# Kernel tuning notes

Hardware: AMD Instinct MI355X
Metric: run time of the kernel (lower is better)

## Reference

```python
import jax, jax.numpy as jnp
import numpy as np

NUM_USER = 100000
NUM_ITEM = 50000
N = NUM_USER + NUM_ITEM
E = 1200000
D = 64          # emb_size
F_ITEM = 384    # raw item multimodal feature dim
K = 3           # number of global embedding rows (summed over dim 0)
N_LAYERS = 4
EPS = 1e-8      # F.cosine_similarity default eps


def setup_inputs() -> dict:
    key = jax.random.key(0)
    ks = jax.random.split(key, 9)
    return {
        "adj_row": jax.random.randint(ks[0], (E,), 0, N),
        "adj_col": jax.random.randint(ks[1], (E,), 0, N),
        # scaled like a degree-normalized adjacency (avg degree ~8)
        "adj_val": jax.random.uniform(ks[2], (E,), jnp.float32) / 8.0,
        "user_fea": jax.random.normal(ks[3], (NUM_USER, D), jnp.float32) * 0.1,
        "item_fea": jax.random.normal(ks[4], (NUM_ITEM, F_ITEM), jnp.float32) * 0.1,
        "g_emb_u": jax.random.normal(ks[5], (K, D), jnp.float32) * 0.1,
        "g_emb_i": jax.random.normal(ks[6], (K, D), jnp.float32) * 0.1,
        "mlp_w": jax.random.normal(ks[7], (D, F_ITEM), jnp.float32) * (1.0 / np.sqrt(F_ITEM)),
        "mlp_b": jnp.zeros((D,), jnp.float32),
    }


def _cosine_sim(a, b):
    # matches F.cosine_similarity(a, b, dim=-1) with eps clamp on norms
    na = jnp.maximum(jnp.linalg.norm(a, axis=-1), EPS)
    nb = jnp.maximum(jnp.linalg.norm(b, axis=-1), EPS)
    return jnp.sum(a * b, axis=-1) / (na * nb)


def reference(adj_row, adj_col, adj_val, user_fea, item_fea, g_emb_u, g_emb_i, mlp_w, mlp_b):
    # global embeddings summed over modality dim
    user_emb = user_fea + jnp.sum(g_emb_u, axis=0)                       # [U, D]
    item_emb = jnp.tanh(item_fea @ mlp_w.T + mlp_b) + jnp.sum(g_emb_i, axis=0)  # [I, D]
    ego = jnp.concatenate([user_emb, item_emb], axis=0)                  # [N, D]

    x = ego
    acc = ego  # sum over layers, includes layer-0 (ego) term
    for _ in range(N_LAYERS):
        # sparse adj @ x as gather -> scale -> segment-sum scatter
        x = jax.ops.segment_sum(adj_val[:, None] * x[adj_col], adj_row, num_segments=N)
        w = _cosine_sim(x, ego)     # [N]
        x = w[:, None] * x          # einsum('a,ab->ab')
        acc = acc + x

    return acc[:NUM_USER], acc[NUM_USER:]
```

## Files before the change

kernel.cpp:

```cpp
#include <hip/hip_runtime.h>
#include <hip/hip_bf16.h>

#define U_NUM 100000
#define I_NUM 50000
#define N_NUM 150000
#define E_NUM 1200000
#define D 64
#define F_IT 384
#define CAP 32
#define EPSV 1e-8f

typedef unsigned short ushort_t;
typedef unsigned int uint_t;
typedef short bf16x8 __attribute__((ext_vector_type(8)));
typedef float f32x4 __attribute__((ext_vector_type(4)));

__device__ __forceinline__ ushort_t f2bf(float f) {
    uint_t x = __float_as_uint(f);
    uint_t r = x + 0x7fffu + ((x >> 16) & 1u);
    return (ushort_t)(r >> 16);
}
__device__ __forceinline__ float bfu2f(uint_t u_lo16) {
    return __uint_as_float(u_lo16 << 16);
}

__global__ void k_zero(int* p, int n) {
    int i = blockIdx.x * 256 + threadIdx.x;
    if (i < n) p[i] = 0;
}

__global__ void k_fill(const int* __restrict__ row, const int* __restrict__ col,
                       const float* __restrict__ val,
                       int* __restrict__ cnt, int2* __restrict__ bkt) {
    int t = blockIdx.x * 256 + threadIdx.x;
    if (t >= E_NUM / 4) return;
    int r[4], c[4];
    float v[4];
#pragma unroll
    for (int k = 0; k < 4; k++) {
        int e = t + k * (E_NUM / 4);
        r[k] = row[e]; c[k] = col[e]; v[k] = val[e];
    }
    int p[4];
#pragma unroll
    for (int k = 0; k < 4; k++) p[k] = atomicAdd(&cnt[r[k]], 1);
#pragma unroll
    for (int k = 0; k < 4; k++) {
        if (p[k] < CAP) bkt[r[k] * CAP + p[k]] = make_int2(c[k], __float_as_int(v[k]));
    }
}

__global__ void k_wcast(const float* __restrict__ w, short* __restrict__ wbf) {
    int i = blockIdx.x * 256 + threadIdx.x;
    wbf[i] = (short)f2bf(w[i]);
}

__global__ void k_user(const float* __restrict__ ufea, const float* __restrict__ gu,
                       float* __restrict__ ego, ushort_t* __restrict__ egob) {
    int i = blockIdx.x * 256 + threadIdx.x;
    int d = i & 63;
    float g = gu[d] + gu[64 + d] + gu[128 + d];
    float v = ufea[i] + g;
    ego[i] = v;
    egob[i] = f2bf(v);
}

__global__ __launch_bounds__(256) void k_item(const float* __restrict__ ifea,
                                              const short* __restrict__ wbf,
                                              const float* __restrict__ b,
                                              const float* __restrict__ gi,
                                              float* __restrict__ ego,
                                              ushort_t* __restrict__ egob) {
    int wave = threadIdx.x >> 6;
    int lane = threadIdx.x & 63;
    int q = lane >> 4, m = lane & 15;
    int ibase = blockIdx.x * 64 + wave * 16;

    int irow = min(ibase + m, I_NUM - 1);
    const float* arow = ifea + (size_t)irow * F_IT + q * 8;

    f32x4 av[4];
#pragma unroll
    for (int n = 0; n < 4; n++) av[n] = (f32x4){0.f, 0.f, 0.f, 0.f};

#pragma unroll
    for (int c = 0; c < 12; c++) {
        float4 fa0 = ((const float4*)(arow + c * 32))[0];
        float4 fa1 = ((const float4*)(arow + c * 32))[1];
        bf16x8 af;
        af[0] = (short)f2bf(fa0.x); af[1] = (short)f2bf(fa0.y);
        af[2] = (short)f2bf(fa0.z); af[3] = (short)f2bf(fa0.w);
        af[4] = (short)f2bf(fa1.x); af[5] = (short)f2bf(fa1.y);
        af[6] = (short)f2bf(fa1.z); af[7] = (short)f2bf(fa1.w);
#pragma unroll
        for (int n = 0; n < 4; n++) {
            bf16x8 bf = *(const bf16x8*)(wbf + (size_t)(n * 16 + m) * F_IT + c * 32 + q * 8);
            av[n] = __builtin_amdgcn_mfma_f32_16x16x32_bf16(af, bf, av[n], 0, 0, 0);
        }
    }

#pragma unroll
    for (int n = 0; n < 4; n++) {
        int dim = n * 16 + m;
        float bb = b[dim];
        float gg = gi[dim] + gi[64 + dim] + gi[128 + dim];
#pragma unroll
        for (int r = 0; r < 4; r++) {
            int item = ibase + q * 4 + r;
            if (item < I_NUM) {
                float v = tanhf(av[n][r] + bb) + gg;
                size_t o = (size_t)(U_NUM + item) * D + dim;
                ego[o] = v;
                egob[o] = f2bf(v);
            }
        }
    }
}

__global__ void k_norm(const float* __restrict__ ego, float* __restrict__ nrm) {
    int t = blockIdx.x * 256 + threadIdx.x;
    int r = t >> 4, l = t & 15;
    float4 e = ((const float4*)ego)[r * 16 + l];
    float s = e.x * e.x + e.y * e.y + e.z * e.z + e.w * e.w;
    s += __shfl_xor(s, 1);
    s += __shfl_xor(s, 2);
    s += __shfl_xor(s, 4);
    s += __shfl_xor(s, 8);
    if (l == 0) nrm[r] = fmaxf(sqrtf(s), EPSV);
}

__global__ __launch_bounds__(256) void k_spmm(const ushort_t* __restrict__ xb,
                                              const ushort_t* __restrict__ egob,
                                              const float* __restrict__ nrm,
                                              const int* __restrict__ cnt,
                                              const int2* __restrict__ bkt,
                                              ushort_t* __restrict__ xob) {
    int t = blockIdx.x * 256 + threadIdx.x;
    int r = t >> 3, l = t & 7;
    if (r >= N_NUM) return;
    int deg = min(cnt[r], CAP);
    const int2* bp = bkt + (size_t)r * CAP;

    int2 eb0 = bp[l], eb1 = bp[l + 8], eb2 = bp[l + 16], eb3 = bp[l + 24];

    float a[8];
#pragma unroll
    for (int j = 0; j < 8; j++) a[j] = 0.f;

    int nch = (deg + 7) >> 3;
    for (int k = 0; k < nch; k++) {
        int2 e = (k == 0) ? eb0 : (k == 1) ? eb1 : (k == 2) ? eb2 : eb3;
#pragma unroll
        for (int j = 0; j < 8; j++) {
            int cc = __shfl(e.x, j, 8);
            int vi = __shfl(e.y, j, 8);
            bool act = (k * 8 + j) < deg;
            float v = act ? __int_as_float(vi) : 0.f;
            cc = act ? cc : 0;
            uint4 xv = ((const uint4*)xb)[(size_t)cc * 8 + l];
            a[0] += v * bfu2f(xv.x & 0xffffu); a[1] += v * bfu2f(xv.x >> 16);
            a[2] += v * bfu2f(xv.y & 0xffffu); a[3] += v * bfu2f(xv.y >> 16);
            a[4] += v * bfu2f(xv.z & 0xffffu); a[5] += v * bfu2f(xv.z >> 16);
            a[6] += v * bfu2f(xv.w & 0xffffu); a[7] += v * bfu2f(xv.w >> 16);
        }
    }

    uint4 ev = ((const uint4*)egob)[(size_t)r * 8 + l];
    float dot = a[0] * bfu2f(ev.x & 0xffffu) + a[1] * bfu2f(ev.x >> 16)
              + a[2] * bfu2f(ev.y & 0xffffu) + a[3] * bfu2f(ev.y >> 16)
              + a[4] * bfu2f(ev.z & 0xffffu) + a[5] * bfu2f(ev.z >> 16)
              + a[6] * bfu2f(ev.w & 0xffffu) + a[7] * bfu2f(ev.w >> 16);
    float nx = a[0] * a[0] + a[1] * a[1] + a[2] * a[2] + a[3] * a[3]
             + a[4] * a[4] + a[5] * a[5] + a[6] * a[6] + a[7] * a[7];
    dot += __shfl_xor(dot, 1); nx += __shfl_xor(nx, 1);
    dot += __shfl_xor(dot, 2); nx += __shfl_xor(nx, 2);
    dot += __shfl_xor(dot, 4); nx += __shfl_xor(nx, 4);
    float wgt = dot / (fmaxf(sqrtf(nx), EPSV) * nrm[r]);

    uint4 ov;
    ov.x = (uint_t)f2bf(wgt * a[0]) | ((uint_t)f2bf(wgt * a[1]) << 16);
    ov.y = (uint_t)f2bf(wgt * a[2]) | ((uint_t)f2bf(wgt * a[3]) << 16);
    ov.z = (uint_t)f2bf(wgt * a[4]) | ((uint_t)f2bf(wgt * a[5]) << 16);
    ov.w = (uint_t)f2bf(wgt * a[6]) | ((uint_t)f2bf(wgt * a[7]) << 16);
    ((uint4*)xob)[(size_t)r * 8 + l] = ov;
}

__global__ void k_out(const float* __restrict__ ego,
                      const ushort_t* __restrict__ x1, const ushort_t* __restrict__ x2,
                      const ushort_t* __restrict__ x3, const ushort_t* __restrict__ x4,
                      float* __restrict__ out) {
    int t = blockIdx.x * 256 + threadIdx.x;
    if (t >= N_NUM * 8) return;
    size_t b = (size_t)t * 8;
    float4 s0 = ((const float4*)(ego + b))[0];
    float4 s1 = ((const float4*)(ego + b))[1];
    uint4 u1 = ((const uint4*)x1)[t], u2 = ((const uint4*)x2)[t];
    uint4 u3 = ((const uint4*)x3)[t], u4 = ((const uint4*)x4)[t];
#define ADD8(u) \
    s0.x += bfu2f(u.x & 0xffffu); s0.y += bfu2f(u.x >> 16); \
    s0.z += bfu2f(u.y & 0xffffu); s0.w += bfu2f(u.y >> 16); \
    s1.x += bfu2f(u.z & 0xffffu); s1.y += bfu2f(u.z >> 16); \
    s1.z += bfu2f(u.w & 0xffffu); s1.w += bfu2f(u.w >> 16);
    ADD8(u1) ADD8(u2) ADD8(u3) ADD8(u4)
#undef ADD8
    ((float4*)(out + b))[0] = s0;
    ((float4*)(out + b))[1] = s1;
}

extern "C" void kernel_launch(void* const* d_in, const int* in_sizes, int n_in,
                              void* d_out, int out_size, void* d_ws, size_t ws_size,
                              hipStream_t stream) {
    const int*   adj_row  = (const int*)d_in[0];
    const int*   adj_col  = (const int*)d_in[1];
    const float* adj_val  = (const float*)d_in[2];
    const float* user_fea = (const float*)d_in[3];
    const float* item_fea = (const float*)d_in[4];
    const float* gu       = (const float*)d_in[5];
    const float* gi       = (const float*)d_in[6];
    const float* mlp_w    = (const float*)d_in[7];
    const float* mlp_b    = (const float*)d_in[8];

    float* out = (float*)d_out;

    char* ws = (char*)d_ws;
    size_t off = 0;
    float*    ego  = (float*)(ws + off);    off += (size_t)N_NUM * D * 4;
    ushort_t* egob = (ushort_t*)(ws + off); off += (size_t)N_NUM * D * 2;
    ushort_t* x1   = (ushort_t*)(ws + off); off += (size_t)N_NUM * D * 2;
    ushort_t* x2   = (ushort_t*)(ws + off); off += (size_t)N_NUM * D * 2;
    ushort_t* x3   = (ushort_t*)(ws + off); off += (size_t)N_NUM * D * 2;
    ushort_t* x4   = (ushort_t*)(ws + off); off += (size_t)N_NUM * D * 2;
    float*    nrm  = (float*)(ws + off);    off += (size_t)N_NUM * 4;
    int*      cnt  = (int*)(ws + off);      off += (size_t)N_NUM * 4;
    short*    wbf  = (short*)(ws + off);    off += (size_t)D * F_IT * 2;
    off = (off + 255) & ~(size_t)255;
    int2*     bkt  = (int2*)(ws + off);     off += (size_t)N_NUM * CAP * 8;

    k_zero<<<(N_NUM + 255) / 256, 256, 0, stream>>>(cnt, N_NUM);
    k_fill<<<(E_NUM / 4 + 255) / 256, 256, 0, stream>>>(adj_row, adj_col, adj_val, cnt, bkt);
    k_wcast<<<D * F_IT / 256, 256, 0, stream>>>(mlp_w, wbf);
    k_user<<<U_NUM * D / 256, 256, 0, stream>>>(user_fea, gu, ego, egob);
    k_item<<<(I_NUM + 63) / 64, 256, 0, stream>>>(item_fea, wbf, mlp_b, gi, ego, egob);
    k_norm<<<N_NUM * 16 / 256, 256, 0, stream>>>(ego, nrm);

    int g = (N_NUM * 8 + 255) / 256;
    k_spmm<<<g, 256, 0, stream>>>(egob, egob, nrm, cnt, bkt, x1);
    k_spmm<<<g, 256, 0, stream>>>(x1,   egob, nrm, cnt, bkt, x2);
    k_spmm<<<g, 256, 0, stream>>>(x2,   egob, nrm, cnt, bkt, x3);
    k_spmm<<<g, 256, 0, stream>>>(x3,   egob, nrm, cnt, bkt, x4);

    k_out<<<g, 256, 0, stream>>>(ego, x1, x2, x3, x4, out);
}
```

Measured before the change: 429.6 us.

## Fuse setup kernels, process two rows per SpMM group, fuse final layer with output

Setup work is merged: k_prep zeroes the counters, casts the weights and presums the global embeddings, and k_mega interleaves edge bucketing, the item MLP and the user embedding in one launch. The separate norm kernel is removed, and the ego norm is now recomputed inside each SpMM. Each 8-lane group handles two rows to expose more independent gathers, and accumulation uses fixed-point integer adds, which is exact in order but risks overflow or quantization error. The last SpMM layer is fused with the output sum, which removes the x4 buffer and the k_out pass.

```diff
diff --git a/kernel.cpp b/kernel.cpp
--- a/kernel.cpp
+++ b/kernel.cpp
@@ -9,6 +9,8 @@
 #define F_IT 384
 #define CAP 32
 #define EPSV 1e-8f
+#define FXS 524288.0f
+#define FXI (1.0f / 524288.0f)
 
 typedef unsigned short ushort_t;
 typedef unsigned int uint_t;
@@ -23,188 +25,283 @@
 __device__ __forceinline__ float bfu2f(uint_t u_lo16) {
     return __uint_as_float(u_lo16 << 16);
 }
-
-__global__ void k_zero(int* p, int n) {
-    int i = blockIdx.x * 256 + threadIdx.x;
-    if (i < n) p[i] = 0;
-}
-
-__global__ void k_fill(const int* __restrict__ row, const int* __restrict__ col,
-                       const float* __restrict__ val,
-                       int* __restrict__ cnt, int2* __restrict__ bkt) {
-    int t = blockIdx.x * 256 + threadIdx.x;
-    if (t >= E_NUM / 4) return;
-    int r[4], c[4];
-    float v[4];
-#pragma unroll
-    for (int k = 0; k < 4; k++) {
-        int e = t + k * (E_NUM / 4);
-        r[k] = row[e]; c[k] = col[e]; v[k] = val[e];
-    }
-    int p[4];
-#pragma unroll
-    for (int k = 0; k < 4; k++) p[k] = atomicAdd(&cnt[r[k]], 1);
-#pragma unroll
-    for (int k = 0; k < 4; k++) {
-        if (p[k] < CAP) bkt[r[k] * CAP + p[k]] = make_int2(c[k], __float_as_int(v[k]));
-    }
-}
-
-__global__ void k_wcast(const float* __restrict__ w, short* __restrict__ wbf) {
-    int i = blockIdx.x * 256 + threadIdx.x;
-    wbf[i] = (short)f2bf(w[i]);
-}
-
-__global__ void k_user(const float* __restrict__ ufea, const float* __restrict__ gu,
-                       float* __restrict__ ego, ushort_t* __restrict__ egob) {
-    int i = blockIdx.x * 256 + threadIdx.x;
-    int d = i & 63;
-    float g = gu[d] + gu[64 + d] + gu[128 + d];
-    float v = ufea[i] + g;
-    ego[i] = v;
-    egob[i] = f2bf(v);
-}
-
-__global__ __launch_bounds__(256) void k_item(const float* __restrict__ ifea,
-                                              const short* __restrict__ wbf,
-                                              const float* __restrict__ b,
-                                              const float* __restrict__ gi,
-                                              float* __restrict__ ego,
-                                              ushort_t* __restrict__ egob) {
-    int wave = threadIdx.x >> 6;
-    int lane = threadIdx.x & 63;
-    int q = lane >> 4, m = lane & 15;
-    int ibase = blockIdx.x * 64 + wave * 16;
-
-    int irow = min(ibase + m, I_NUM - 1);
-    const float* arow = ifea + (size_t)irow * F_IT + q * 8;
-
-    f32x4 av[4];
-#pragma unroll
-    for (int n = 0; n < 4; n++) av[n] = (f32x4){0.f, 0.f, 0.f, 0.f};
-
-#pragma unroll
-    for (int c = 0; c < 12; c++) {
-        float4 fa0 = ((const float4*)(arow + c * 32))[0];
-        float4 fa1 = ((const float4*)(arow + c * 32))[1];
-        bf16x8 af;
-        af[0] = (short)f2bf(fa0.x); af[1] = (short)f2bf(fa0.y);
-        af[2] = (short)f2bf(fa0.z); af[3] = (short)f2bf(fa0.w);
-        af[4] = (short)f2bf(fa1.x); af[5] = (short)f2bf(fa1.y);
-        af[6] = (short)f2bf(fa1.z); af[7] = (short)f2bf(fa1.w);
+__device__ __forceinline__ void dec8(uint4 u, float* f) {
+    f[0] = bfu2f(u.x & 0xffffu); f[1] = bfu2f(u.x >> 16);
+    f[2] = bfu2f(u.y & 0xffffu); f[3] = bfu2f(u.y >> 16);
+    f[4] = bfu2f(u.z & 0xffffu); f[5] = bfu2f(u.z >> 16);
+    f[6] = bfu2f(u.w & 0xffffu); f[7] = bfu2f(u.w >> 16);
+}
+
+__global__ void k_prep(const float* __restrict__ w, const float* __restrict__ gu,
+                       const float* __restrict__ gi,
+                       int* __restrict__ cnt, short* __restrict__ wbf,
+                       float* __restrict__ gsu, float* __restrict__ gsi) {
+    int b = blockIdx.x, t = threadIdx.x;
+    if (b < 586) {
+        int i = b * 256 + t;
+        if (i < N_NUM) cnt[i] = 0;
+    } else if (b < 682) {
+        int i = (b - 586) * 256 + t;
+        wbf[i] = (short)f2bf(w[i]);
+    } else {
+        if (t < 64) gsu[t] = gu[t] + gu[64 + t] + gu[128 + t];
+        else if (t < 128) { int d = t - 64; gsi[d] = gi[d] + gi[64 + d] + gi[128 + d]; }
+    }
+}
+
+#define FILL_B 1172
+#define ITEM_B 782
+#define USER_B 1563
+
+__global__ __launch_bounds__(256) void k_mega(
+        const int* __restrict__ row, const int* __restrict__ col,
+        const float* __restrict__ val,
+        const float* __restrict__ ufea, const float* __restrict__ ifea,
+        const float* __restrict__ bvec,
+        const short* __restrict__ wbf,
+        const float* __restrict__ gsu, const float* __restrict__ gsi,
+        int* __restrict__ cnt, int2* __restrict__ bkt,
+        float* __restrict__ ego, ushort_t* __restrict__ egob) {
+    int b = blockIdx.x;
+    int grp = b / 9, slot = b % 9;
+    int tid = threadIdx.x;
+
+    if (slot < 3) {
+        int fid = grp * 3 + slot;
+        if (fid >= FILL_B) return;
+        int t = fid * 256 + tid;
+        if (t >= E_NUM / 4) return;
+        int r[4], c[4];
+        float v[4];
+#pragma unroll
+        for (int k = 0; k < 4; k++) {
+            int e = t + k * (E_NUM / 4);
+            r[k] = row[e]; c[k] = col[e]; v[k] = val[e];
+        }
+        int p[4];
+#pragma unroll
+        for (int k = 0; k < 4; k++) p[k] = atomicAdd(&cnt[r[k]], 1);
+#pragma unroll
+        for (int k = 0; k < 4; k++) {
+            if (p[k] < CAP) bkt[r[k] * CAP + p[k]] = make_int2(c[k], __float_as_int(v[k]));
+        }
+    } else if (slot < 5) {
+        int iid = grp * 2 + (slot - 3);
+        if (iid >= ITEM_B) return;
+        int wave = tid >> 6, lane = tid & 63;
+        int q = lane >> 4, m = lane & 15;
+        int ibase = iid * 64 + wave * 16;
+        int irow = min(ibase + m, I_NUM - 1);
+        const float* arow = ifea + (size_t)irow * F_IT + q * 8;
+
+        f32x4 av[4];
+#pragma unroll
+        for (int n = 0; n < 4; n++) av[n] = (f32x4){0.f, 0.f, 0.f, 0.f};
+#pragma unroll
+        for (int c = 0; c < 12; c++) {
+            float4 fa0 = ((const float4*)(arow + c * 32))[0];
+            float4 fa1 = ((const float4*)(arow + c * 32))[1];
+            bf16x8 af;
+            af[0] = (short)f2bf(fa0.x); af[1] = (short)f2bf(fa0.y);
+            af[2] = (short)f2bf(fa0.z); af[3] = (short)f2bf(fa0.w);
+            af[4] = (short)f2bf(fa1.x); af[5] = (short)f2bf(fa1.y);
+            af[6] = (short)f2bf(fa1.z); af[7] = (short)f2bf(fa1.w);
+#pragma unroll
+            for (int n = 0; n < 4; n++) {
+                bf16x8 bf = *(const bf16x8*)(wbf + (size_t)(n * 16 + m) * F_IT + c * 32 + q * 8);
+                av[n] = __builtin_amdgcn_mfma_f32_16x16x32_bf16(af, bf, av[n], 0, 0, 0);
+            }
+        }
 #pragma unroll
         for (int n = 0; n < 4; n++) {
-            bf16x8 bf = *(const bf16x8*)(wbf + (size_t)(n * 16 + m) * F_IT + c * 32 + q * 8);
-            av[n] = __builtin_amdgcn_mfma_f32_16x16x32_bf16(af, bf, av[n], 0, 0, 0);
-        }
-    }
-
-#pragma unroll
-    for (int n = 0; n < 4; n++) {
-        int dim = n * 16 + m;
-        float bb = b[dim];
-        float gg = gi[dim] + gi[64 + dim] + gi[128 + dim];
-#pragma unroll
-        for (int r = 0; r < 4; r++) {
-            int item = ibase + q * 4 + r;
-            if (item < I_NUM) {
-                float v = tanhf(av[n][r] + bb) + gg;
-                size_t o = (size_t)(U_NUM + item) * D + dim;
-                ego[o] = v;
-                egob[o] = f2bf(v);
+            int dim = n * 16 + m;
+            float bb = bvec[dim];
+            float gg = gsi[dim];
+#pragma unroll
+            for (int rr = 0; rr < 4; rr++) {
+                int item = ibase + q * 4 + rr;
+                if (item < I_NUM) {
+                    float v = tanhf(av[n][rr] + bb) + gg;
+                    size_t o = (size_t)(U_NUM + item) * D + dim;
+                    ego[o] = v;
+                    egob[o] = f2bf(v);
+                }
             }
         }
-    }
-}
-
-__global__ void k_norm(const float* __restrict__ ego, float* __restrict__ nrm) {
-    int t = blockIdx.x * 256 + threadIdx.x;
-    int r = t >> 4, l = t & 15;
-    float4 e = ((const float4*)ego)[r * 16 + l];
-    float s = e.x * e.x + e.y * e.y + e.z * e.z + e.w * e.w;
-    s += __shfl_xor(s, 1);
-    s += __shfl_xor(s, 2);
-    s += __shfl_xor(s, 4);
-    s += __shfl_xor(s, 8);
-    if (l == 0) nrm[r] = fmaxf(sqrtf(s), EPSV);
+    } else {
+        int uid = grp * 4 + (slot - 5);
+        if (uid >= USER_B) return;
+        int t = uid * 256 + tid;
+        size_t base = (size_t)t * 16;
+        if (base >= (size_t)U_NUM * D) return;
+        int d0 = (int)(base & 63);
+        float f[16];
+#pragma unroll
+        for (int k = 0; k < 4; k++) {
+            float4 v = ((const float4*)(ufea + base))[k];
+            f[4 * k] = v.x; f[4 * k + 1] = v.y; f[4 * k + 2] = v.z; f[4 * k + 3] = v.w;
+        }
+#pragma unroll
+        for (int j = 0; j < 16; j++) f[j] += gsu[d0 + j];
+#pragma unroll
+        for (int k = 0; k < 4; k++) {
+            ((float4*)(ego + base))[k] = make_float4(f[4 * k], f[4 * k + 1], f[4 * k + 2], f[4 * k + 3]);
+        }
+        uint4 u0, u1;
+        u0.x = (uint_t)f2bf(f[0]) | ((uint_t)f2bf(f[1]) << 16);
+        u0.y = (uint_t)f2bf(f[2]) | ((uint_t)f2bf(f[3]) << 16);
+        u0.z = (uint_t)f2bf(f[4]) | ((uint_t)f2bf(f[5]) << 16);
+        u0.w = (uint_t)f2bf(f[6]) | ((uint_t)f2bf(f[7]) << 16);
+        u1.x = (uint_t)f2bf(f[8]) | ((uint_t)f2bf(f[9]) << 16);
+        u1.y = (uint_t)f2bf(f[10]) | ((uint_t)f2bf(f[11]) << 16);
+        u1.z = (uint_t)f2bf(f[12]) | ((uint_t)f2bf(f[13]) << 16);
+        u1.w = (uint_t)f2bf(f[14]) | ((uint_t)f2bf(f[15]) << 16);
+        ((uint4*)(egob + base))[0] = u0;
+        ((uint4*)(egob + base))[1] = u1;
+    }
+}
+
+#define ACC8(A, VS, X) \
+    A[0] += __float2int_rn(VS * bfu2f(X.x & 0xffffu)); A[1] += __float2int_rn(VS * bfu2f(X.x >> 16)); \
+    A[2] += __float2int_rn(VS * bfu2f(X.y & 0xffffu)); A[3] += __float2int_rn(VS * bfu2f(X.y >> 16)); \
+    A[4] += __float2int_rn(VS * bfu2f(X.z & 0xffffu)); A[5] += __float2int_rn(VS * bfu2f(X.z >> 16)); \
+    A[6] += __float2int_rn(VS * bfu2f(X.w & 0xffffu)); A[7] += __float2int_rn(VS * bfu2f(X.w >> 16));
+
+__device__ __forceinline__ float row_weight(const float* a, const float* e) {
+    float dot = 0.f, nx = 0.f, ne = 0.f;
+#pragma unroll
+    for (int j = 0; j < 8; j++) {
+        dot += a[j] * e[j]; nx += a[j] * a[j]; ne += e[j] * e[j];
+    }
+#pragma unroll
+    for (int m = 1; m < 8; m <<= 1) {
+        dot += __shfl_xor(dot, m);
+        nx  += __shfl_xor(nx, m);
+        ne  += __shfl_xor(ne, m);
+    }
+    return dot / (fmaxf(sqrtf(nx), EPSV) * fmaxf(sqrtf(ne), EPSV));
 }
 
 __global__ __launch_bounds__(256) void k_spmm(const ushort_t* __restrict__ xb,
                                               const ushort_t* __restrict__ egob,
-                                              const float* __restrict__ nrm,
                                               const int* __restrict__ cnt,
                                               const int2* __restrict__ bkt,
                                               ushort_t* __restrict__ xob) {
     int t = blockIdx.x * 256 + threadIdx.x;
-    int r = t >> 3, l = t & 7;
-    if (r >= N_NUM) return;
-    int deg = min(cnt[r], CAP);
-    const int2* bp = bkt + (size_t)r * CAP;
-
-    int2 eb0 = bp[l], eb1 = bp[l + 8], eb2 = bp[l + 16], eb3 = bp[l + 24];
-
-    float a[8];
-#pragma unroll
-    for (int j = 0; j < 8; j++) a[j] = 0.f;
-
-    int nch = (deg + 7) >> 3;
-    for (int k = 0; k < nch; k++) {
-        int2 e = (k == 0) ? eb0 : (k == 1) ? eb1 : (k == 2) ? eb2 : eb3;
-#pragma unroll
-        for (int j = 0; j < 8; j++) {
-            int cc = __shfl(e.x, j, 8);
-            int vi = __shfl(e.y, j, 8);
-            bool act = (k * 8 + j) < deg;
-            float v = act ? __int_as_float(vi) : 0.f;
-            cc = act ? cc : 0;
-            uint4 xv = ((const uint4*)xb)[(size_t)cc * 8 + l];
-            a[0] += v * bfu2f(xv.x & 0xffffu); a[1] += v * bfu2f(xv.x >> 16);
-            a[2] += v * bfu2f(xv.y & 0xffffu); a[3] += v * bfu2f(xv.y >> 16);
-            a[4] += v * bfu2f(xv.z & 0xffffu); a[5] += v * bfu2f(xv.z >> 16);
-            a[6] += v * bfu2f(xv.w & 0xffffu); a[7] += v * bfu2f(xv.w >> 16);
-        }
-    }
-
-    uint4 ev = ((const uint4*)egob)[(size_t)r * 8 + l];
-    float dot = a[0] * bfu2f(ev.x & 0xffffu) + a[1] * bfu2f(ev.x >> 16)
-              + a[2] * bfu2f(ev.y & 0xffffu) + a[3] * bfu2f(ev.y >> 16)
-              + a[4] * bfu2f(ev.z & 0xffffu) + a[5] * bfu2f(ev.z >> 16)
-              + a[6] * bfu2f(ev.w & 0xffffu) + a[7] * bfu2f(ev.w >> 16);
-    float nx = a[0] * a[0] + a[1] * a[1] + a[2] * a[2] + a[3] * a[3]
-             + a[4] * a[4] + a[5] * a[5] + a[6] * a[6] + a[7] * a[7];
-    dot += __shfl_xor(dot, 1); nx += __shfl_xor(nx, 1);
-    dot += __shfl_xor(dot, 2); nx += __shfl_xor(nx, 2);
-    dot += __shfl_xor(dot, 4); nx += __shfl_xor(nx, 4);
-    float wgt = dot / (fmaxf(sqrtf(nx), EPSV) * nrm[r]);
-
-    uint4 ov;
-    ov.x = (uint_t)f2bf(wgt * a[0]) | ((uint_t)f2bf(wgt * a[1]) << 16);
-    ov.y = (uint_t)f2bf(wgt * a[2]) | ((uint_t)f2bf(wgt * a[3]) << 16);
-    ov.z = (uint_t)f2bf(wgt * a[4]) | ((uint_t)f2bf(wgt * a[5]) << 16);
-    ov.w = (uint_t)f2bf(wgt * a[6]) | ((uint_t)f2bf(wgt * a[7]) << 16);
-    ((uint4*)xob)[(size_t)r * 8 + l] = ov;
-}
-
-__global__ void k_out(const float* __restrict__ ego,
-                      const ushort_t* __restrict__ x1, const ushort_t* __restrict__ x2,
-                      const ushort_t* __restrict__ x3, const ushort_t* __restrict__ x4,
-                      float* __restrict__ out) {
+    int l = t & 7, g = t >> 3;
+    if (g >= N_NUM / 2) return;
+    int r0 = g * 2, r1 = r0 + 1;
+    int deg0 = min(cnt[r0], CAP), deg1 = min(cnt[r1], CAP);
+    const int2* bp0 = bkt + (size_t)r0 * CAP;
+    const int2* bp1 = bkt + (size_t)r1 * CAP;
+    int2 p0[4] = {bp0[l], bp0[l + 8], bp0[l + 16], bp0[l + 24]};
+    int2 p1[4] = {bp1[l], bp1[l + 8], bp1[l + 16], bp1[l + 24]};
+    int a0[8], a1[8];
+#pragma unroll
+    for (int j = 0; j < 8; j++) { a0[j] = 0; a1[j] = 0; }
+    int dmax = max(deg0, deg1);
+#pragma unroll
+    for (int k = 0; k < 4; k++) {
+        if (k * 8 < dmax) {
+            int c0x = p0[k].x, c0y = p0[k].y, c1x = p1[k].x, c1y = p1[k].y;
+#pragma unroll
+            for (int j = 0; j < 8; j++) {
+                int cc0 = __shfl(c0x, j, 8);
+                float v0 = __int_as_float(__shfl(c0y, j, 8));
+                if ((k * 8 + j) >= deg0) { cc0 = 0; v0 = 0.f; }
+                uint4 xv = ((const uint4*)xb)[(size_t)cc0 * 8 + l];
+                int cc1 = __shfl(c1x, j, 8);
+                float v1 = __int_as_float(__shfl(c1y, j, 8));
+                if ((k * 8 + j) >= deg1) { cc1 = 0; v1 = 0.f; }
+                uint4 yv = ((const uint4*)xb)[(size_t)cc1 * 8 + l];
+                float vs0 = v0 * FXS, vs1 = v1 * FXS;
+                ACC8(a0, vs0, xv);
+                ACC8(a1, vs1, yv);
+            }
+        }
+    }
+#pragma unroll
+    for (int rr = 0; rr < 2; rr++) {
+        int r = rr ? r1 : r0;
+        const int* ai = rr ? a1 : a0;
+        float a[8];
+#pragma unroll
+        for (int j = 0; j < 8; j++) a[j] = (float)ai[j] * FXI;
+        float e[8]; dec8(((const uint4*)egob)[(size_t)r * 8 + l], e);
+        float wgt = row_weight(a, e);
+        uint4 ov;
+        ov.x = (uint_t)f2bf(wgt * a[0]) | ((uint_t)f2bf(wgt * a[1]) << 16);
+        ov.y = (uint_t)f2bf(wgt * a[2]) | ((uint_t)f2bf(wgt * a[3]) << 16);
+        ov.z = (uint_t)f2bf(wgt * a[4]) | ((uint_t)f2bf(wgt * a[5]) << 16);
+        ov.w = (uint_t)f2bf(wgt * a[6]) | ((uint_t)f2bf(wgt * a[7]) << 16);
+        ((uint4*)xob)[(size_t)r * 8 + l] = ov;
+    }
+}
+
+__global__ __launch_bounds__(256) void k_spmm4(const ushort_t* __restrict__ x3,
+                                               const ushort_t* __restrict__ x1,
+                                               const ushort_t* __restrict__ x2,
+                                               const float* __restrict__ ego,
+                                               const int* __restrict__ cnt,
+                                               const int2* __restrict__ bkt,
+                                               float* __restrict__ out) {
     int t = blockIdx.x * 256 + threadIdx.x;
-    if (t >= N_NUM * 8) return;
-    size_t b = (size_t)t * 8;
-    float4 s0 = ((const float4*)(ego + b))[0];
-    float4 s1 = ((const float4*)(ego + b))[1];
-    uint4 u1 = ((const uint4*)x1)[t], u2 = ((const uint4*)x2)[t];
-    uint4 u3 = ((const uint4*)x3)[t], u4 = ((const uint4*)x4)[t];
-#define ADD8(u) \
-    s0.x += bfu2f(u.x & 0xffffu); s0.y += bfu2f(u.x >> 16); \
-    s0.z += bfu2f(u.y & 0xffffu); s0.w += bfu2f(u.y >> 16); \
-    s1.x += bfu2f(u.z & 0xffffu); s1.y += bfu2f(u.z >> 16); \
-    s1.z += bfu2f(u.w & 0xffffu); s1.w += bfu2f(u.w >> 16);
-    ADD8(u1) ADD8(u2) ADD8(u3) ADD8(u4)
-#undef ADD8
-    ((float4*)(out + b))[0] = s0;
-    ((float4*)(out + b))[1] = s1;
+    int l = t & 7, g = t >> 3;
+    if (g >= N_NUM / 2) return;
+    int r0 = g * 2, r1 = r0 + 1;
+    int deg0 = min(cnt[r0], CAP), deg1 = min(cnt[r1], CAP);
+    const int2* bp0 = bkt + (size_t)r0 * CAP;
+    const int2* bp1 = bkt + (size_t)r1 * CAP;
+    int2 p0[4] = {bp0[l], bp0[l + 8], bp0[l + 16], bp0[l + 24]};
+    int2 p1[4] = {bp1[l], bp1[l + 8], bp1[l + 16], bp1[l + 24]};
+    int a0[8], a1[8];
+#pragma unroll
+    for (int j = 0; j < 8; j++) { a0[j] = 0; a1[j] = 0; }
+    int dmax = max(deg0, deg1);
+#pragma unroll
+    for (int k = 0; k < 4; k++) {
+        if (k * 8 < dmax) {
+            int c0x = p0[k].x, c0y = p0[k].y, c1x = p1[k].x, c1y = p1[k].y;
+#pragma unroll
+            for (int j = 0; j < 8; j++) {
+                int cc0 = __shfl(c0x, j, 8);
+                float v0 = __int_as_float(__shfl(c0y, j, 8));
+                if ((k * 8 + j) >= deg0) { cc0 = 0; v0 = 0.f; }
+                uint4 xv = ((const uint4*)x3)[(size_t)cc0 * 8 + l];
+                int cc1 = __shfl(c1x, j, 8);
+                float v1 = __int_as_float(__shfl(c1y, j, 8));
+                if ((k * 8 + j) >= deg1) { cc1 = 0; v1 = 0.f; }
+                uint4 yv = ((const uint4*)x3)[(size_t)cc1 * 8 + l];
+                float vs0 = v0 * FXS, vs1 = v1 * FXS;
+                ACC8(a0, vs0, xv);
+                ACC8(a1, vs1, yv);
+            }
+        }
+    }
+#pragma unroll
+    for (int rr = 0; rr < 2; rr++) {
+        int r = rr ? r1 : r0;
+        const int* ai = rr ? a1 : a0;
+        float a[8];
+#pragma unroll
+        for (int j = 0; j < 8; j++) a[j] = (float)ai[j] * FXI;
+        size_t rb = (size_t)r * D + l * 8;
+        float e[8];
+        float4 e0 = ((const float4*)(ego + rb))[0];
+        float4 e1 = ((const float4*)(ego + rb))[1];
+        e[0] = e0.x; e[1] = e0.y; e[2] = e0.z; e[3] = e0.w;
+        e[4] = e1.x; e[5] = e1.y; e[6] = e1.z; e[7] = e1.w;
+        float wgt = row_weight(a, e);
+        float s[8];
+        float x1d[8], x2d[8], x3d[8];
+        dec8(((const uint4*)x1)[(size_t)r * 8 + l], x1d);
+        dec8(((const uint4*)x2)[(size_t)r * 8 + l], x2d);
+        dec8(((const uint4*)x3)[(size_t)r * 8 + l], x3d);
+#pragma unroll
+        for (int j = 0; j < 8; j++) s[j] = e[j] + x1d[j] + x2d[j] + x3d[j] + wgt * a[j];
+        ((float4*)(out + rb))[0] = make_float4(s[0], s[1], s[2], s[3]);
+        ((float4*)(out + rb))[1] = make_float4(s[4], s[5], s[6], s[7]);
+    }
 }
 
 extern "C" void kernel_launch(void* const* d_in, const int* in_sizes, int n_in,
@@ -229,25 +326,19 @@
     ushort_t* x1   = (ushort_t*)(ws + off); off += (size_t)N_NUM * D * 2;
     ushort_t* x2   = (ushort_t*)(ws + off); off += (size_t)N_NUM * D * 2;
     ushort_t* x3   = (ushort_t*)(ws + off); off += (size_t)N_NUM * D * 2;
-    ushort_t* x4   = (ushort_t*)(ws + off); off += (size_t)N_NUM * D * 2;
-    float*    nrm  = (float*)(ws + off);    off += (size_t)N_NUM * 4;
     int*      cnt  = (int*)(ws + off);      off += (size_t)N_NUM * 4;
     short*    wbf  = (short*)(ws + off);    off += (size_t)D * F_IT * 2;
+    float*    gsu  = (float*)(ws + off);    off += 64 * 4;
+    float*    gsi  = (float*)(ws + off);    off += 64 * 4;
     off = (off + 255) & ~(size_t)255;
     int2*     bkt  = (int2*)(ws + off);     off += (size_t)N_NUM * CAP * 8;
 
-    k_zero<<<(N_NUM + 255) / 256, 256, 0, stream>>>(cnt, N_NUM);
-    k_fill<<<(E_NUM / 4 + 255) / 256, 256, 0, stream>>>(adj_row, adj_col, adj_val, cnt, bkt);
-    k_wcast<<<D * F_IT / 256, 256, 0, stream>>>(mlp_w, wbf);
-    k_user<<<U_NUM * D / 256, 256, 0, stream>>>(user_fea, gu, ego, egob);
-    k_item<<<(I_NUM + 63) / 64, 256, 0, stream>>>(item_fea, wbf, mlp_b, gi, ego, egob);
-    k_norm<<<N_NUM * 16 / 256, 256, 0, stream>>>(ego, nrm);
-
-    int g = (N_NUM * 8 + 255) / 256;
-    k_spmm<<<g, 256, 0, stream>>>(egob, egob, nrm, cnt, bkt, x1);
-    k_spmm<<<g, 256, 0, stream>>>(x1,   egob, nrm, cnt, bkt, x2);
-    k_spmm<<<g, 256, 0, stream>>>(x2,   egob, nrm, cnt, bkt, x3);
-    k_spmm<<<g, 256, 0, stream>>>(x3,   egob, nrm, cnt, bkt, x4);
-
-    k_out<<<g, 256, 0, stream>>>(ego, x1, x2, x3, x4, out);
-}
+    k_prep<<<683, 256, 0, stream>>>(mlp_w, gu, gi, cnt, wbf, gsu, gsi);
+    k_mega<<<391 * 9, 256, 0, stream>>>(adj_row, adj_col, adj_val, user_fea, item_fea,
+                                        mlp_b, wbf, gsu, gsi, cnt, bkt, ego, egob);
+    int g = (N_NUM / 2 * 8 + 255) / 256;
+    k_spmm<<<g, 256, 0, stream>>>(egob, egob, cnt, bkt, x1);
+    k_spmm<<<g, 256, 0, stream>>>(x1,   egob, cnt, bkt, x2);
+    k_spmm<<<g, 256, 0, stream>>>(x2,   egob, cnt, bkt, x3);
+    k_spmm4<<<g, 256, 0, stream>>>(x3, x1, x2, ego, cnt, bkt, out);
+}
```

New measurement: 409.9 us. 4.6% less time.
